# Kernel optimization log

Hardware: AMD Instinct MI355X
Metric: run time of the kernel (lower is better)

## Reference

```python
import jax, jax.numpy as jnp
import numpy as np

TOP_K = 8      # num_activated_experts
ALPHA = 0.01   # aux_loss_alpha (training mode, seq_aux=False)


def setup_inputs() -> dict:
    key = jax.random.key(0)
    k1, k2 = jax.random.split(key)
    B, S, D, E = 2, 8192, 4096, 64
    hidden_states = jax.random.normal(k1, (B, S, D), dtype=jnp.float32)
    # nn.Parameter(torch.randn(E, D) / sqrt(D))
    weight = jax.random.normal(k2, (E, D), dtype=jnp.float32) / np.float32(np.sqrt(D))
    return {"hidden_states": hidden_states, "weight": weight}


def reference(hidden_states, weight):
    B, S, D = hidden_states.shape
    E = weight.shape[0]
    x = hidden_states.reshape(-1, D)                      # [N, D], N = B*S tokens
    logits = jnp.einsum('nd,ed->ne', x, weight)           # F.linear, no bias
    scores = jax.nn.softmax(logits, axis=-1)              # [N, E]
    topk_weight, topk_idx = jax.lax.top_k(scores, TOP_K)  # [N, K] (torch uses sorted=False; same set)
    # top_k > 1 and norm_topk_prob=False -> no renormalization
    # aux loss (training, seq_aux=False): ce = mean one-hot load, pi = mean scores
    flat_idx = topk_idx.reshape(-1)                       # [N*K]
    ce = jnp.zeros((E,), scores.dtype).at[flat_idx].add(1.0) / flat_idx.size
    pi = scores.mean(axis=0)                              # [E]
    aux_loss = jnp.sum(pi * ce * E) * jnp.asarray(ALPHA, scores.dtype)
    return topk_idx, topk_weight, aux_loss
```

## Files before the change

### kernel.cpp

```cpp
#include <hip/hip_runtime.h>
#include <math.h>

#define DDIM 4096
#define NEXP 64

typedef short s16x8 __attribute__((ext_vector_type(8)));
typedef float f32x4 __attribute__((ext_vector_type(4)));

__device__ __forceinline__ unsigned cvt_pk_bf16(float a, float b) {
  unsigned r;
  asm("v_cvt_pk_bf16_f32 %0, %1, %2" : "=v"(r) : "v"(a), "v"(b));
  return r;
}

__device__ __forceinline__ void split2(float a, float b, unsigned& H,
                                       unsigned& M, unsigned& L) {
  H = cvt_pk_bf16(a, b);
  float h0 = __uint_as_float(H << 16);
  float h1 = __uint_as_float(H & 0xffff0000u);
  float r0 = a - h0, r1 = b - h1;
  M = cvt_pk_bf16(r0, r1);
  float m0 = __uint_as_float(M << 16);
  float m1 = __uint_as_float(M & 0xffff0000u);
  L = cvt_pk_bf16(r0 - m0, r1 - m1);
}

union U8 { unsigned u[4]; s16x8 v; };
__device__ __forceinline__ s16x8 pack8(const unsigned* a) {
  U8 t;
  t.u[0] = a[0]; t.u[1] = a[1]; t.u[2] = a[2]; t.u[3] = a[3];
  return t.v;
}

__device__ __forceinline__ void stage3(const ushort* __restrict__ wf, int kb,
                                       char* dst, int sw, int lane) {
#pragma unroll
  for (int j = 0; j < 3; ++j) {
    const int c = sw * 3 + j;
    __builtin_amdgcn_global_load_lds(
        (const __attribute__((address_space(1))) void*)(wf + (size_t)(kb * 12 + c) * 512 + lane * 8),
        (__attribute__((address_space(3))) void*)(dst + c * 1024), 16, 0, 0);
  }
}

#define MFMA(A, B, C) __builtin_amdgcn_mfma_f32_16x16x32_bf16(A, B, C, 0, 0, 0)

__global__ __launch_bounds__(1024) void moe_gate_main(
    const float* __restrict__ x,
    const ushort* __restrict__ wf,
    float* __restrict__ out,
    float* __restrict__ pi_g, float* __restrict__ ce_g, int N) {
  __shared__ float smem[24576];
  float* lt = smem;
  float* inv_s = smem + 17408;
  float* ce_lds = smem + 17472;

  const int tid = threadIdx.x;
  const int lane = tid & 63;
  const int wv = tid >> 6;
  const int g = wv >> 2;
  const int sw = wv & 3;
  const int tok0 = blockIdx.x << 6;
  const int rot = ((blockIdx.x * 9) + (g << 3)) & 31;

  char* gbuf = (char*)smem + g * 24576;
  const float* xr = x + (size_t)(tok0 + (sw << 4) + (lane & 15)) * DDIM +
                    (g << 10) + ((lane >> 4) << 3);
  const ushort* wfg = wf + (size_t)g * 32 * 12 * 512;

  f32x4 accH[4], accC[4];
#pragma unroll
  for (int eg = 0; eg < 4; ++eg) {
#pragma unroll
    for (int r = 0; r < 4; ++r) { accH[eg][r] = 0.f; accC[eg][r] = 0.f; }
  }

  const int p1 = (rot + 1) & 31, p2 = (rot + 2) & 31, p3 = (rot + 3) & 31;
  stage3(wfg, rot, gbuf, sw, lane);
  asm volatile("" ::: "memory");
  float4 x0a = ((const float4*)(xr + rot * 32))[0];
  float4 x0b = ((const float4*)(xr + rot * 32))[1];
  float4 x1a = ((const float4*)(xr + p1 * 32))[0];
  float4 x1b = ((const float4*)(xr + p1 * 32))[1];
  asm volatile("" ::: "memory");
  stage3(wfg, p1, gbuf + 12288, sw, lane);
  asm volatile("" ::: "memory");
  float4 x2a = ((const float4*)(xr + p2 * 32))[0];
  float4 x2b = ((const float4*)(xr + p2 * 32))[1];
  float4 x3a = ((const float4*)(xr + p3 * 32))[0];
  float4 x3b = ((const float4*)(xr + p3 * 32))[1];
  asm volatile("" ::: "memory");

#define GBODY(XA, XB, PAR, I)                                                  \
  {                                                                            \
    asm volatile("s_waitcnt vmcnt(7)" ::: "memory");                           \
    __builtin_amdgcn_s_barrier();                                              \
    unsigned AH[4], AM[4], AL[4];                                              \
    split2(XA.x, XA.y, AH[0], AM[0], AL[0]);                                   \
    split2(XA.z, XA.w, AH[1], AM[1], AL[1]);                                   \
    split2(XB.x, XB.y, AH[2], AM[2], AL[2]);                                   \
    split2(XB.z, XB.w, AH[3], AM[3], AL[3]);                                   \
    s16x8 ah = pack8(AH), am = pack8(AM), al = pack8(AL);                      \
    const char* bb = gbuf + (PAR)*12288 + lane * 16;                           \
    _Pragma("unroll") for (int eg = 0; eg < 4; ++eg) {                         \
      s16x8 bh = *(const s16x8*)(bb + (eg * 3 + 0) * 1024);                    \
      s16x8 bm = *(const s16x8*)(bb + (eg * 3 + 1) * 1024);                    \
      s16x8 bl = *(const s16x8*)(bb + (eg * 3 + 2) * 1024);                    \
      accH[eg] = MFMA(ah, bh, accH[eg]);                                       \
      accC[eg] = MFMA(ah, bm, accC[eg]);                                       \
      accC[eg] = MFMA(am, bh, accC[eg]);                                       \
      accC[eg] = MFMA(am, bm, accC[eg]);                                       \
      accC[eg] = MFMA(ah, bl, accC[eg]);                                       \
      accC[eg] = MFMA(al, bh, accC[eg]);                                       \
    }                                                                          \
    __builtin_amdgcn_s_barrier();                                              \
    asm volatile("" ::: "memory");                                             \
    stage3(wfg, ((I) + 2 + rot) & 31, gbuf + (PAR)*12288, sw, lane);           \
    asm volatile("" ::: "memory");                                             \
    {                                                                          \
      const int kn = ((I) + 4 + rot) & 31;                                     \
      XA = ((const float4*)(xr + kn * 32))[0];                                 \
      XB = ((const float4*)(xr + kn * 32))[1];                                 \
    }                                                                          \
    asm volatile("" ::: "memory");                                             \
  }

#pragma unroll 1
  for (int i = 0; i < 32; i += 4) {
    GBODY(x0a, x0b, 0, i);
    GBODY(x1a, x1b, 1, i + 1);
    GBODY(x2a, x2b, 0, i + 2);
    GBODY(x3a, x3b, 1, i + 3);
  }

  asm volatile("s_waitcnt vmcnt(0)" ::: "memory");
  __syncthreads();

  {
    float* ltp = smem + g * 4352;
#pragma unroll
    for (int eg = 0; eg < 4; ++eg) {
#pragma unroll
      for (int r = 0; r < 4; ++r) {
        ltp[(eg * 16 + (lane & 15)) * 68 + (sw << 4) + ((lane >> 4) << 2) + r] =
            accH[eg][r] + accC[eg][r];
      }
    }
  }
  __syncthreads();

  for (int idx = tid; idx < 4352; idx += 1024)
    lt[idx] = (lt[idx] + smem[4352 + idx] + smem[8704 + idx] + smem[13056 + idx]) * 0.015625f;
  __syncthreads();

  if (tid < 64) {
    const int t = tid;
    ce_lds[t] = 0.f;
    float m = -1e30f;
#pragma unroll 1
    for (int e = 0; e < 64; ++e) m = fmaxf(m, lt[e * 68 + t]);
    float ssum = 0.f;
#pragma unroll 1
    for (int e = 0; e < 64; ++e) {
      float p = expf(lt[e * 68 + t] - m);
      lt[e * 68 + t] = p;
      ssum += p;
    }
    inv_s[t] = 1.f / ssum;
  }
  __syncthreads();

  if (tid < 64) {
    const int e = tid;
    float ssum = 0.f;
#pragma unroll 1
    for (int t = 0; t < 64; ++t) ssum += lt[e * 68 + t] * inv_s[t];
    atomicAdd(pi_g + e, ssum);
  }
  __syncthreads();

  if (tid < 64) {
    const int t = tid;
    const float invv = inv_s[t];
    const size_t tg = (size_t)(tok0 + t);
#pragma unroll 1
    for (int r = 0; r < 8; ++r) {
      float bv = -1.f;
      int bi = 0;
#pragma unroll 1
      for (int e = 0; e < 64; ++e) {
        float p = lt[e * 68 + t];
        if (p > bv) { bv = p; bi = e; }
      }
      lt[bi * 68 + t] = -1.f;
      atomicAdd(ce_lds + bi, 1.f);
      out[tg * 8 + r] = (float)bi;
      out[(size_t)N * 8 + tg * 8 + r] = bv * invv;
    }
  }
  __syncthreads();
  if (tid < 64) atomicAdd(ce_g + tid, ce_lds[tid]);
}

__global__ void build_wfrag(const float* __restrict__ w, ushort* __restrict__ wf) {
  const int kb = blockIdx.x;
  const int t = threadIdx.x;
  const int eg = t >> 6, lane = t & 63;
  const int e = (eg << 4) + (lane & 15);
  const int k0 = (kb << 5) + ((lane >> 4) << 3);
  const float* src = w + (size_t)e * DDIM + k0;
  unsigned H[4], M[4], L[4];
#pragma unroll
  for (int i = 0; i < 4; ++i) {
    float a = src[2 * i] * 64.f, b = src[2 * i + 1] * 64.f;
    split2(a, b, H[i], M[i], L[i]);
  }
  const size_t base = ((size_t)kb * 12 + eg * 3) * 512 + (size_t)lane * 8;
  *(uint4*)(wf + base) = make_uint4(H[0], H[1], H[2], H[3]);
  *(uint4*)(wf + base + 512) = make_uint4(M[0], M[1], M[2], M[3]);
  *(uint4*)(wf + base + 1024) = make_uint4(L[0], L[1], L[2], L[3]);
}

__global__ void aux_final(const float* __restrict__ pi_g,
                          const float* __restrict__ ce_g,
                          float* __restrict__ out_aux, int N) {
  const int e = threadIdx.x;
  float v = (pi_g[e] / (float)N) * (ce_g[e] / ((float)N * 8.0f)) * 64.0f * 0.01f;
#pragma unroll
  for (int off = 32; off; off >>= 1) v += __shfl_down(v, off, 64);
  if (e == 0) *out_aux = v;
}

extern "C" void kernel_launch(void* const* d_in, const int* in_sizes, int n_in,
                              void* d_out, int out_size, void* d_ws, size_t ws_size,
                              hipStream_t stream) {
  (void)n_in; (void)out_size; (void)ws_size;
  const float* x = (const float*)d_in[0];
  const float* w = (const float*)d_in[1];
  float* out = (float*)d_out;
  const int N = in_sizes[0] / DDIM;

  ushort* wf = (ushort*)d_ws;
  float* pi_g = (float*)((char*)d_ws + (size_t)128 * 12 * 512 * 2);
  float* ce_g = pi_g + 64;

  hipMemsetAsync(pi_g, 0, 128 * sizeof(float), stream);
  build_wfrag<<<128, 256, 0, stream>>>(w, wf);
  moe_gate_main<<<N / 64, 1024, 0, stream>>>(x, wf, out, pi_g, ce_g, N);
  aux_final<<<1, 64, 0, stream>>>(pi_g, ce_g, out + (size_t)N * 16, N);
}
```

Baseline: 118.0 us.

## Load weight fragments directly from global memory instead of LDS staging

Drops the double-buffered global_load_lds staging of the split bf16 weight fragments, along with its per-step vmcnt waits and workgroup barriers. Each wave now reads its B fragments straight from global memory, relying on the cache to serve the small shared weight array. LDS shrinks to what the epilogue needs. The cost is that the four waves of a group each fetch the same weight data, which multiplies L1/L2 traffic. There is also no explicit prefetch of weights ahead of the MFMAs that consume them.

```diff
diff --git a/kernel.cpp b/kernel.cpp
--- a/kernel.cpp
+++ b/kernel.cpp
@@ -32,17 +32,6 @@
   return t.v;
 }
 
-__device__ __forceinline__ void stage3(const ushort* __restrict__ wf, int kb,
-                                       char* dst, int sw, int lane) {
-#pragma unroll
-  for (int j = 0; j < 3; ++j) {
-    const int c = sw * 3 + j;
-    __builtin_amdgcn_global_load_lds(
-        (const __attribute__((address_space(1))) void*)(wf + (size_t)(kb * 12 + c) * 512 + lane * 8),
-        (__attribute__((address_space(3))) void*)(dst + c * 1024), 16, 0, 0);
-  }
-}
-
 #define MFMA(A, B, C) __builtin_amdgcn_mfma_f32_16x16x32_bf16(A, B, C, 0, 0, 0)
 
 __global__ __launch_bounds__(1024) void moe_gate_main(
@@ -50,7 +39,7 @@
     const ushort* __restrict__ wf,
     float* __restrict__ out,
     float* __restrict__ pi_g, float* __restrict__ ce_g, int N) {
-  __shared__ float smem[24576];
+  __shared__ float smem[17536];
   float* lt = smem;
   float* inv_s = smem + 17408;
   float* ce_lds = smem + 17472;
@@ -63,7 +52,6 @@
   const int tok0 = blockIdx.x << 6;
   const int rot = ((blockIdx.x * 9) + (g << 3)) & 31;
 
-  char* gbuf = (char*)smem + g * 24576;
   const float* xr = x + (size_t)(tok0 + (sw << 4) + (lane & 15)) * DDIM +
                     (g << 10) + ((lane >> 4) << 3);
   const ushort* wfg = wf + (size_t)g * 32 * 12 * 512;
@@ -76,36 +64,34 @@
   }
 
   const int p1 = (rot + 1) & 31, p2 = (rot + 2) & 31, p3 = (rot + 3) & 31;
-  stage3(wfg, rot, gbuf, sw, lane);
-  asm volatile("" ::: "memory");
   float4 x0a = ((const float4*)(xr + rot * 32))[0];
   float4 x0b = ((const float4*)(xr + rot * 32))[1];
   float4 x1a = ((const float4*)(xr + p1 * 32))[0];
   float4 x1b = ((const float4*)(xr + p1 * 32))[1];
-  asm volatile("" ::: "memory");
-  stage3(wfg, p1, gbuf + 12288, sw, lane);
-  asm volatile("" ::: "memory");
   float4 x2a = ((const float4*)(xr + p2 * 32))[0];
   float4 x2b = ((const float4*)(xr + p2 * 32))[1];
   float4 x3a = ((const float4*)(xr + p3 * 32))[0];
   float4 x3b = ((const float4*)(xr + p3 * 32))[1];
-  asm volatile("" ::: "memory");
-
-#define GBODY(XA, XB, PAR, I)                                                  \
+
+#define KSTEP(XA, XB, I)                                                       \
   {                                                                            \
-    asm volatile("s_waitcnt vmcnt(7)" ::: "memory");                           \
-    __builtin_amdgcn_s_barrier();                                              \
+    const int kb = ((I) + rot) & 31;                                           \
     unsigned AH[4], AM[4], AL[4];                                              \
     split2(XA.x, XA.y, AH[0], AM[0], AL[0]);                                   \
     split2(XA.z, XA.w, AH[1], AM[1], AL[1]);                                   \
     split2(XB.x, XB.y, AH[2], AM[2], AL[2]);                                   \
     split2(XB.z, XB.w, AH[3], AM[3], AL[3]);                                   \
-    s16x8 ah = pack8(AH), am = pack8(AM), al = pack8(AL);                      \
-    const char* bb = gbuf + (PAR)*12288 + lane * 16;                           \
+    const s16x8 ah = pack8(AH), am = pack8(AM), al = pack8(AL);                \
+    {                                                                          \
+      const int kn = ((I) + 4 + rot) & 31;                                     \
+      XA = ((const float4*)(xr + kn * 32))[0];                                 \
+      XB = ((const float4*)(xr + kn * 32))[1];                                 \
+    }                                                                          \
+    const ushort* wk = wfg + (size_t)kb * (12 * 512) + lane * 8;               \
     _Pragma("unroll") for (int eg = 0; eg < 4; ++eg) {                         \
-      s16x8 bh = *(const s16x8*)(bb + (eg * 3 + 0) * 1024);                    \
-      s16x8 bm = *(const s16x8*)(bb + (eg * 3 + 1) * 1024);                    \
-      s16x8 bl = *(const s16x8*)(bb + (eg * 3 + 2) * 1024);                    \
+      const s16x8 bh = *(const s16x8*)(wk + (eg * 3 + 0) * 512);               \
+      const s16x8 bm = *(const s16x8*)(wk + (eg * 3 + 1) * 512);               \
+      const s16x8 bl = *(const s16x8*)(wk + (eg * 3 + 2) * 512);               \
       accH[eg] = MFMA(ah, bh, accH[eg]);                                       \
       accC[eg] = MFMA(ah, bm, accC[eg]);                                       \
       accC[eg] = MFMA(am, bh, accC[eg]);                                       \
@@ -113,28 +99,15 @@
       accC[eg] = MFMA(ah, bl, accC[eg]);                                       \
       accC[eg] = MFMA(al, bh, accC[eg]);                                       \
     }                                                                          \
-    __builtin_amdgcn_s_barrier();                                              \
-    asm volatile("" ::: "memory");                                             \
-    stage3(wfg, ((I) + 2 + rot) & 31, gbuf + (PAR)*12288, sw, lane);           \
-    asm volatile("" ::: "memory");                                             \
-    {                                                                          \
-      const int kn = ((I) + 4 + rot) & 31;                                     \
-      XA = ((const float4*)(xr + kn * 32))[0];                                 \
-      XB = ((const float4*)(xr + kn * 32))[1];                                 \
-    }                                                                          \
-    asm volatile("" ::: "memory");                                             \
   }
 
 #pragma unroll 1
   for (int i = 0; i < 32; i += 4) {
-    GBODY(x0a, x0b, 0, i);
-    GBODY(x1a, x1b, 1, i + 1);
-    GBODY(x2a, x2b, 0, i + 2);
-    GBODY(x3a, x3b, 1, i + 3);
-  }
-
-  asm volatile("s_waitcnt vmcnt(0)" ::: "memory");
-  __syncthreads();
+    KSTEP(x0a, x0b, i);
+    KSTEP(x1a, x1b, i + 1);
+    KSTEP(x2a, x2b, i + 2);
+    KSTEP(x3a, x3b, i + 3);
+  }
 
   {
     float* ltp = smem + g * 4352;
@@ -182,7 +155,7 @@
   if (tid < 64) {
     const int t = tid;
     const float invv = inv_s[t];
-    const size_t tg = (size_t)(tok0 + t);
+    const size_t tg2 = (size_t)(tok0 + t);
 #pragma unroll 1
     for (int r = 0; r < 8; ++r) {
       float bv = -1.f;
@@ -194,8 +167,8 @@
       }
       lt[bi * 68 + t] = -1.f;
       atomicAdd(ce_lds + bi, 1.f);
-      out[tg * 8 + r] = (float)bi;
-      out[(size_t)N * 8 + tg * 8 + r] = bv * invv;
+      out[tg2 * 8 + r] = (float)bi;
+      out[(size_t)N * 8 + tg2 * 8 + r] = bv * invv;
     }
   }
   __syncthreads();
```

After: 143.5 us. 1.22x slower.
